# Performance work log

Measured on AMD Instinct MI355X. Metric: run time of the kernel, lower is better.

Reference implementation:

```python
import jax, jax.numpy as jnp
import numpy as np

K = 3  # number of nearest neighbors for interpolation
BIG = 1e10  # masks out cross-batch pairs in the distance matrix


def setup_inputs() -> dict:
    key = jax.random.key(0)
    ks = jax.random.split(key, 8)
    N, Ns, C, Cs, B = 4096, 16384, 256, 128, 4
    Din, H = C + Cs, 256
    return {
        "x": jax.random.normal(ks[0], (N, C), dtype=jnp.float32),
        "pos": jax.random.normal(ks[1], (N, 3), dtype=jnp.float32),
        "batch": jnp.sort(jax.random.randint(ks[2], (N,), 0, B)),
        "x_skip": jax.random.normal(ks[3], (Ns, Cs), dtype=jnp.float32),
        "pos_skip": jax.random.normal(ks[4], (Ns, 3), dtype=jnp.float32),
        "batch_skip": jnp.sort(jax.random.randint(ks[5], (Ns,), 0, B)),
        "W1": jax.random.normal(ks[6], (Din, H), dtype=jnp.float32) * (1.0 / np.sqrt(Din)),
        "b1": jnp.zeros((H,), dtype=jnp.float32),
        "W2": jax.random.normal(ks[7], (H, H), dtype=jnp.float32) * (1.0 / np.sqrt(H)),
        "b2": jnp.zeros((H,), dtype=jnp.float32),
    }


def reference(x, pos, batch, x_skip, pos_skip, batch_skip, W1, b1, W2, b2):
    # knn_interpolate: squared distances from each fine point to all coarse points,
    # masked so neighbors only come from the same batch element.
    d2 = jnp.sum((pos_skip[:, None, :] - pos[None, :, :]) ** 2, axis=-1)  # [Ns, N]
    d2 = jnp.where(batch_skip[:, None] != batch[None, :], BIG, d2)
    neg_d2, idx = jax.lax.top_k(-d2, K)          # k smallest distances, [Ns, K]
    w = 1.0 / jnp.clip(-neg_d2, 1e-16)           # inverse-squared-distance weights
    num = jnp.sum(x[idx] * w[..., None], axis=1)  # [Ns, C] weighted gather-reduce
    y = num / jnp.sum(w, axis=1, keepdims=True)
    # concat skip features, then MLP (Linear-ReLU-Linear-ReLU)
    y = jnp.concatenate([y, x_skip], axis=1)      # [Ns, C + Cs]
    h = jax.nn.relu(y @ W1 + b1)
    out = jax.nn.relu(h @ W2 + b2)
    return (out, pos_skip, batch_skip)
```

## Files before the change

### kernel.cpp

```cpp
#include <hip/hip_runtime.h>
#include <stdint.h>

#define NPTS   4096
#define NSKIP  16384
#define CCH    256
#define CSK    128
#define DIN    384
#define HDIM   256
#define BIGF   1e10f

typedef unsigned short u16;
typedef __attribute__((ext_vector_type(8))) short short8;
typedef __attribute__((ext_vector_type(4))) float floatx4;

__device__ __forceinline__ u16 f2bf(float f) {
    union { float f; uint32_t u; } c; c.f = f;
    uint32_t u = c.u;
    return (u16)((u + 0x7FFFu + ((u >> 16) & 1u)) >> 16);
}

__device__ __forceinline__ double pkkey(float d, int j) {
    return __hiloint2double(__float_as_int(d), j);
}

__global__ __launch_bounds__(256) void prep_knn_kernel(
    const float* __restrict__ W1, const float* __restrict__ W2,
    u16* __restrict__ W1p, u16* __restrict__ W2p,
    const float* __restrict__ pos, const int* __restrict__ batch,
    const float* __restrict__ pos_skip, const int* __restrict__ batch_skip,
    int* __restrict__ idx3, float* __restrict__ w3)
{
    const int bid = blockIdx.x;
    const int t = threadIdx.x;

    if (bid < 80) {
        const float* W = (bid < 48) ? W1 : W2;
        u16* Wp       = (bid < 48) ? W1p : W2p;
        const int KT  = (bid < 48) ? 12 : 8;
        const int g   = ((bid < 48) ? bid : (bid - 48)) * 256 + t;

        const int lane = g & 63;
        const int kt = (g >> 6) % KT;
        const int nt = (g >> 6) / KT;
        const int kbase = kt * 32 + (lane >> 4) * 8;
        const int n = nt * 16 + (lane & 15);
        u16 v[8];
#pragma unroll
        for (int j = 0; j < 8; ++j) v[j] = f2bf(W[(size_t)(kbase + j) * HDIM + n]);
#pragma unroll
        for (int j = 0; j < 8; ++j) Wp[(size_t)g * 8 + j] = v[j];
        return;
    }

    __shared__ int sRange[5];
    if (t < 5) {
        int lo = 0, hi = NPTS;
        while (lo < hi) {
            const int m = (lo + hi) >> 1;
            if (batch[m] < t) lo = m + 1; else hi = m;
        }
        sRange[t] = lo;
    }
    __syncthreads();

    const int i = (bid - 80) * 8 + (t >> 5);
    const int sub = t & 31;
    const int b = batch_skip[i];
    const int start = sRange[b], end = sRange[b + 1];

    const float px = pos_skip[i * 3 + 0];
    const float py = pos_skip[i * 3 + 1];
    const float pz = pos_skip[i * 3 + 2];

    const double BIGKEY = pkkey(BIGF, 0x7FFFFFFF);
    double k0 = BIGKEY, k1 = BIGKEY, k2 = BIGKEY;

    for (int j = start + sub; j < end; j += 32) {
        const float qx = pos[j * 3 + 0];
        const float qy = pos[j * 3 + 1];
        const float qz = pos[j * 3 + 2];
        const float dx = __fsub_rn(px, qx);
        const float dy = __fsub_rn(py, qy);
        const float dz = __fsub_rn(pz, qz);
        const float dd = __fadd_rn(__fadd_rn(__fmul_rn(dx, dx), __fmul_rn(dy, dy)),
                                   __fmul_rn(dz, dz));
        const double kk = pkkey(dd, j);
        const double u0 = fmax(k0, kk); k0 = fmin(k0, kk);
        const double u1 = fmax(k1, u0); k1 = fmin(k1, u0);
        k2 = fmin(k2, u1);
    }

#pragma unroll
    for (int m = 1; m < 32; m <<= 1) {
        const double o0 = __shfl_xor(k0, m);
        const double o1 = __shfl_xor(k1, m);
        const double o2 = __shfl_xor(k2, m);
        double u0 = fmax(k0, o0); k0 = fmin(k0, o0);
        double u1 = fmax(k1, u0); k1 = fmin(k1, u0);
        k2 = fmin(k2, u1);
        u1 = fmax(k1, o1); k1 = fmin(k1, o1);
        k2 = fmin(k2, u1);
        k2 = fmin(k2, o2);
    }

    if (sub == 0) {
        const float d0 = __int_as_float(__double2hiint(k0));
        const float d1 = __int_as_float(__double2hiint(k1));
        const float d2 = __int_as_float(__double2hiint(k2));
        const float w0 = 1.0f / fmaxf(d0, 1e-16f);
        const float w1 = 1.0f / fmaxf(d1, 1e-16f);
        const float w2 = 1.0f / fmaxf(d2, 1e-16f);
        const float inv = 1.0f / (w0 + w1 + w2);
        idx3[i * 3 + 0] = __double2loint(k0);
        idx3[i * 3 + 1] = __double2loint(k1);
        idx3[i * 3 + 2] = __double2loint(k2);
        w3[i * 3 + 0] = w0 * inv; w3[i * 3 + 1] = w1 * inv; w3[i * 3 + 2] = w2 * inv;
    }
}

__global__ __launch_bounds__(256) void fused_mlp_kernel(
    const float* __restrict__ x, const float* __restrict__ x_skip,
    const int* __restrict__ idx3, const float* __restrict__ w3,
    const u16* __restrict__ W1p, const float* __restrict__ b1,
    const u16* __restrict__ W2p, const float* __restrict__ b2,
    const float* __restrict__ pos_skip, const int* __restrict__ batch_skip,
    float* __restrict__ out)
{
    __shared__ u16 sA[32 * 392];
    const int t = threadIdx.x;
    const int row0 = blockIdx.x * 32;

#pragma unroll
    for (int k = 0; k < 8; ++k) {
        const int g = t + 256 * k;
        const int row = g >> 6, c4 = g & 63;
        const int R = row0 + row;
        const int i0 = idx3[R * 3 + 0], i1 = idx3[R * 3 + 1], i2 = idx3[R * 3 + 2];
        const float w0 = w3[R * 3 + 0], w1 = w3[R * 3 + 1], w2 = w3[R * 3 + 2];
        const float4 v0 = *(const float4*)(x + (size_t)i0 * CCH + c4 * 4);
        const float4 v1 = *(const float4*)(x + (size_t)i1 * CCH + c4 * 4);
        const float4 v2 = *(const float4*)(x + (size_t)i2 * CCH + c4 * 4);
        const float a  = w0 * v0.x + w1 * v1.x + w2 * v2.x;
        const float bq = w0 * v0.y + w1 * v1.y + w2 * v2.y;
        const float cq = w0 * v0.z + w1 * v1.z + w2 * v2.z;
        const float dq = w0 * v0.w + w1 * v1.w + w2 * v2.w;
        uint2 pk;
        pk.x = (uint32_t)f2bf(a)  | ((uint32_t)f2bf(bq) << 16);
        pk.y = (uint32_t)f2bf(cq) | ((uint32_t)f2bf(dq) << 16);
        *(uint2*)(sA + row * 392 + c4 * 4) = pk;
    }
#pragma unroll
    for (int k = 0; k < 4; ++k) {
        const int g = t + 256 * k;
        const int row = g >> 5, c4 = g & 31;
        const float4 v = *(const float4*)(x_skip + (size_t)(row0 + row) * CSK + c4 * 4);
        uint2 pk;
        pk.x = (uint32_t)f2bf(v.x) | ((uint32_t)f2bf(v.y) << 16);
        pk.y = (uint32_t)f2bf(v.z) | ((uint32_t)f2bf(v.w) << 16);
        *(uint2*)(sA + row * 392 + CCH + c4 * 4) = pk;
    }
    __syncthreads();

    const int wave = t >> 6, lane = t & 63;
    const int quad = lane >> 4, ml = lane & 15;

    floatx4 acc[2][4] = {};
    {
        const u16* aA = sA + ml * 392 + quad * 8;
        for (int kt = 0; kt < 12; ++kt) {
            short8 a0 = *(const short8*)(aA + kt * 32);
            short8 a1 = *(const short8*)(aA + 16 * 392 + kt * 32);
#pragma unroll
            for (int nt = 0; nt < 4; ++nt) {
                const int ntile = wave * 4 + nt;
                short8 bfr = *(const short8*)(W1p + (size_t)((ntile * 12 + kt) * 64 + lane) * 8);
                acc[0][nt] = __builtin_amdgcn_mfma_f32_16x16x32_bf16(a0, bfr, acc[0][nt], 0, 0, 0);
                acc[1][nt] = __builtin_amdgcn_mfma_f32_16x16x32_bf16(a1, bfr, acc[1][nt], 0, 0, 0);
            }
        }
    }
    __syncthreads();

#pragma unroll
    for (int mt = 0; mt < 2; ++mt) {
#pragma unroll
        for (int nt = 0; nt < 4; ++nt) {
            const int n = (wave * 4 + nt) * 16 + ml;
            const float bv = b1[n];
#pragma unroll
            for (int r = 0; r < 4; ++r) {
                const int m = mt * 16 + quad * 4 + r;
                sA[m * 264 + n] = f2bf(fmaxf(acc[mt][nt][r] + bv, 0.0f));
            }
        }
    }
    __syncthreads();

    floatx4 acc2[2][4] = {};
    {
        const u16* aH = sA + ml * 264 + quad * 8;
        for (int kt = 0; kt < 8; ++kt) {
            short8 a0 = *(const short8*)(aH + kt * 32);
            short8 a1 = *(const short8*)(aH + 16 * 264 + kt * 32);
#pragma unroll
            for (int nt = 0; nt < 4; ++nt) {
                const int ntile = wave * 4 + nt;
                short8 bfr = *(const short8*)(W2p + (size_t)((ntile * 8 + kt) * 64 + lane) * 8);
                acc2[0][nt] = __builtin_amdgcn_mfma_f32_16x16x32_bf16(a0, bfr, acc2[0][nt], 0, 0, 0);
                acc2[1][nt] = __builtin_amdgcn_mfma_f32_16x16x32_bf16(a1, bfr, acc2[1][nt], 0, 0, 0);
            }
        }
    }

#pragma unroll
    for (int mt = 0; mt < 2; ++mt) {
#pragma unroll
        for (int nt = 0; nt < 4; ++nt) {
            const int n = (wave * 4 + nt) * 16 + ml;
            const float bv = b2[n];
#pragma unroll
            for (int r = 0; r < 4; ++r) {
                const int m = row0 + mt * 16 + quad * 4 + r;
                out[(size_t)m * HDIM + n] = fmaxf(acc2[mt][nt][r] + bv, 0.0f);
            }
        }
    }

    if (t < 128) {
        const int e = blockIdx.x * 128 + t;
        const size_t base = (size_t)NSKIP * HDIM;
        if (e < NSKIP * 3) out[base + e] = pos_skip[e];
        else               out[base + e] = (float)batch_skip[e - NSKIP * 3];
    }
}

extern "C" void kernel_launch(void* const* d_in, const int* in_sizes, int n_in,
                              void* d_out, int out_size, void* d_ws, size_t ws_size,
                              hipStream_t stream) {
    const float* x         = (const float*)d_in[0];
    const float* pos       = (const float*)d_in[1];
    const int*   batch     = (const int*)d_in[2];
    const float* x_skip    = (const float*)d_in[3];
    const float* pos_skip  = (const float*)d_in[4];
    const int*   batch_skip= (const int*)d_in[5];
    const float* W1        = (const float*)d_in[6];
    const float* b1        = (const float*)d_in[7];
    const float* W2        = (const float*)d_in[8];
    const float* b2        = (const float*)d_in[9];
    float* out = (float*)d_out;

    char* ws = (char*)d_ws;
    u16*    W1p   = (u16*)ws;
    u16*    W2p   = (u16*)(ws + 196608);
    int*    idx3  = (int*)(ws + 327680);
    float*  w3    = (float*)(ws + 524288);

    prep_knn_kernel<<<80 + NSKIP / 8, 256, 0, stream>>>(W1, W2, W1p, W2p,
                                                        pos, batch,
                                                        pos_skip, batch_skip,
                                                        idx3, w3);
    fused_mlp_kernel<<<NSKIP / 32, 256, 0, stream>>>(x, x_skip, idx3, w3,
                                                     W1p, b1, W2p, b2,
                                                     pos_skip, batch_skip, out);
}
```

Measured before the change: 118.0 us.

## Use 1024-thread MLP blocks with one N-tile per wave and LDS-staged output

The fused MLP kernel now runs 16 waves per block instead of 4. Each wave owns a single 16-column N tile, which shrinks the per-thread accumulators and the gather loops. The final ReLU results go to a new shared-memory buffer and are then written to global memory as coalesced float4 stores, replacing scattered scalar stores. This trades much larger LDS use per block and fewer resident blocks per CU for more waves and better store coalescing.

After: 114.3 us. -3.2%, faster.

```diff
diff --git a/kernel.cpp b/kernel.cpp
--- a/kernel.cpp
+++ b/kernel.cpp
@@ -118,7 +118,7 @@
     }
 }
 
-__global__ __launch_bounds__(256) void fused_mlp_kernel(
+__global__ __launch_bounds__(1024, 8) void fused_mlp_kernel(
     const float* __restrict__ x, const float* __restrict__ x_skip,
     const int* __restrict__ idx3, const float* __restrict__ w3,
     const u16* __restrict__ W1p, const float* __restrict__ b1,
@@ -127,12 +127,15 @@
     float* __restrict__ out)
 {
     __shared__ u16 sA[32 * 392];
+    __shared__ float sOut[32 * 256];
     const int t = threadIdx.x;
     const int row0 = blockIdx.x * 32;
-
-#pragma unroll
-    for (int k = 0; k < 8; ++k) {
-        const int g = t + 256 * k;
+    const int wave = t >> 6, lane = t & 63;
+    const int quad = lane >> 4, ml = lane & 15;
+
+#pragma unroll
+    for (int k = 0; k < 2; ++k) {
+        const int g = t + 1024 * k;
         const int row = g >> 6, c4 = g & 63;
         const int R = row0 + row;
         const int i0 = idx3[R * 3 + 0], i1 = idx3[R * 3 + 1], i2 = idx3[R * 3 + 2];
@@ -149,10 +152,8 @@
         pk.y = (uint32_t)f2bf(cq) | ((uint32_t)f2bf(dq) << 16);
         *(uint2*)(sA + row * 392 + c4 * 4) = pk;
     }
-#pragma unroll
-    for (int k = 0; k < 4; ++k) {
-        const int g = t + 256 * k;
-        const int row = g >> 5, c4 = g & 31;
+    {
+        const int row = t >> 5, c4 = t & 31;
         const float4 v = *(const float4*)(x_skip + (size_t)(row0 + row) * CSK + c4 * 4);
         uint2 pk;
         pk.x = (uint32_t)f2bf(v.x) | ((uint32_t)f2bf(v.y) << 16);
@@ -161,68 +162,64 @@
     }
     __syncthreads();
 
-    const int wave = t >> 6, lane = t & 63;
-    const int quad = lane >> 4, ml = lane & 15;
-
-    floatx4 acc[2][4] = {};
+    floatx4 acc[2] = {};
     {
         const u16* aA = sA + ml * 392 + quad * 8;
         for (int kt = 0; kt < 12; ++kt) {
             short8 a0 = *(const short8*)(aA + kt * 32);
             short8 a1 = *(const short8*)(aA + 16 * 392 + kt * 32);
-#pragma unroll
-            for (int nt = 0; nt < 4; ++nt) {
-                const int ntile = wave * 4 + nt;
-                short8 bfr = *(const short8*)(W1p + (size_t)((ntile * 12 + kt) * 64 + lane) * 8);
-                acc[0][nt] = __builtin_amdgcn_mfma_f32_16x16x32_bf16(a0, bfr, acc[0][nt], 0, 0, 0);
-                acc[1][nt] = __builtin_amdgcn_mfma_f32_16x16x32_bf16(a1, bfr, acc[1][nt], 0, 0, 0);
-            }
-        }
-    }
-    __syncthreads();
-
-#pragma unroll
-    for (int mt = 0; mt < 2; ++mt) {
-#pragma unroll
-        for (int nt = 0; nt < 4; ++nt) {
-            const int n = (wave * 4 + nt) * 16 + ml;
-            const float bv = b1[n];
+            short8 bfr = *(const short8*)(W1p + (size_t)((wave * 12 + kt) * 64 + lane) * 8);
+            acc[0] = __builtin_amdgcn_mfma_f32_16x16x32_bf16(a0, bfr, acc[0], 0, 0, 0);
+            acc[1] = __builtin_amdgcn_mfma_f32_16x16x32_bf16(a1, bfr, acc[1], 0, 0, 0);
+        }
+    }
+    __syncthreads();
+
+    {
+        const int n = wave * 16 + ml;
+        const float bv = b1[n];
+#pragma unroll
+        for (int mt = 0; mt < 2; ++mt) {
 #pragma unroll
             for (int r = 0; r < 4; ++r) {
                 const int m = mt * 16 + quad * 4 + r;
-                sA[m * 264 + n] = f2bf(fmaxf(acc[mt][nt][r] + bv, 0.0f));
+                sA[m * 264 + n] = f2bf(fmaxf(acc[mt][r] + bv, 0.0f));
             }
         }
     }
     __syncthreads();
 
-    floatx4 acc2[2][4] = {};
+    floatx4 acc2[2] = {};
     {
         const u16* aH = sA + ml * 264 + quad * 8;
         for (int kt = 0; kt < 8; ++kt) {
             short8 a0 = *(const short8*)(aH + kt * 32);
             short8 a1 = *(const short8*)(aH + 16 * 264 + kt * 32);
-#pragma unroll
-            for (int nt = 0; nt < 4; ++nt) {
-                const int ntile = wave * 4 + nt;
-                short8 bfr = *(const short8*)(W2p + (size_t)((ntile * 8 + kt) * 64 + lane) * 8);
-                acc2[0][nt] = __builtin_amdgcn_mfma_f32_16x16x32_bf16(a0, bfr, acc2[0][nt], 0, 0, 0);
-                acc2[1][nt] = __builtin_amdgcn_mfma_f32_16x16x32_bf16(a1, bfr, acc2[1][nt], 0, 0, 0);
+            short8 bfr = *(const short8*)(W2p + (size_t)((wave * 8 + kt) * 64 + lane) * 8);
+            acc2[0] = __builtin_amdgcn_mfma_f32_16x16x32_bf16(a0, bfr, acc2[0], 0, 0, 0);
+            acc2[1] = __builtin_amdgcn_mfma_f32_16x16x32_bf16(a1, bfr, acc2[1], 0, 0, 0);
+        }
+    }
+
+    {
+        const int n = wave * 16 + ml;
+        const float bv = b2[n];
+#pragma unroll
+        for (int mt = 0; mt < 2; ++mt) {
+#pragma unroll
+            for (int r = 0; r < 4; ++r) {
+                const int m = mt * 16 + quad * 4 + r;
+                sOut[m * 256 + n] = fmaxf(acc2[mt][r] + bv, 0.0f);
             }
         }
     }
-
-#pragma unroll
-    for (int mt = 0; mt < 2; ++mt) {
-#pragma unroll
-        for (int nt = 0; nt < 4; ++nt) {
-            const int n = (wave * 4 + nt) * 16 + ml;
-            const float bv = b2[n];
-#pragma unroll
-            for (int r = 0; r < 4; ++r) {
-                const int m = row0 + mt * 16 + quad * 4 + r;
-                out[(size_t)m * HDIM + n] = fmaxf(acc2[mt][nt][r] + bv, 0.0f);
-            }
+    __syncthreads();
+    {
+        float* dst = out + (size_t)row0 * HDIM;
+#pragma unroll
+        for (int k = 0; k < 2; ++k) {
+            const int e = t + 1024 * k;
+            *(float4*)(dst + e * 4) = *(const float4*)(sOut + e * 4);
         }
     }
 
@@ -259,7 +256,7 @@
                                                         pos, batch,
                                                         pos_skip, batch_skip,
                                                         idx3, w3);
-    fused_mlp_kernel<<<NSKIP / 32, 256, 0, stream>>>(x, x_skip, idx3, w3,
-                                                     W1p, b1, W2p, b2,
-                                                     pos_skip, batch_skip, out);
-}
+    fused_mlp_kernel<<<NSKIP / 32, 1024, 0, stream>>>(x, x_skip, idx3, w3,
+                                                      W1p, b1, W2p, b2,
+                                                      pos_skip, batch_skip, out);
+}
```
